# Optimization experiments

Measured on AMD Instinct MI355X. Metric: run time of the kernel, lower is better.

## Reference

```python
import jax, jax.numpy as jnp
import numpy as np

N_NODES = 50000
N_EDGES = 800000
DIM = 128
BN_EPS = 1e-5  # torch.nn.BatchNorm1d default


def _lin_init(k, fan_in, fan_out):
    kw, kb = jax.random.split(k)
    s = 1.0 / np.sqrt(fan_in)
    W = jax.random.uniform(kw, (fan_in, fan_out), jnp.float32, -s, s)
    b = jax.random.uniform(kb, (fan_out,), jnp.float32, -s, s)
    return W, b


def setup_inputs() -> dict:
    key = jax.random.key(0)
    ks = jax.random.split(key, 8)
    d = {}
    d['h'] = jax.random.normal(ks[0], (N_NODES, DIM), jnp.float32)
    d['e'] = jax.random.normal(ks[1], (N_EDGES, DIM), jnp.float32)
    d['src'] = jax.random.randint(ks[2], (N_EDGES,), 0, N_NODES)
    d['dst'] = jax.random.randint(ks[3], (N_EDGES,), 0, N_NODES)
    # mlp_atom: Linear(128,128) -> ReLU -> Linear(128,128)
    d['Wa1'], d['ba1'] = _lin_init(ks[4], DIM, DIM)
    d['Wa2'], d['ba2'] = _lin_init(ks[5], DIM, DIM)
    # mlp_bond
    d['Wb1'], d['bb1'] = _lin_init(ks[6], DIM, DIM)
    d['Wb2'], d['bb2'] = _lin_init(ks[7], DIM, DIM)
    # BatchNorm1d affine params
    d['gamma_a'] = jnp.ones((DIM,), jnp.float32)
    d['beta_a'] = jnp.zeros((DIM,), jnp.float32)
    d['gamma_b'] = jnp.ones((DIM,), jnp.float32)
    d['beta_b'] = jnp.zeros((DIM,), jnp.float32)
    return d


def _mlp(x, W1, b1, W2, b2):
    return jax.nn.relu(x @ W1 + b1) @ W2 + b2


def _bn(x, gamma, beta):
    # training-mode batch norm over the node/edge axis
    mu = jnp.mean(x, axis=0)
    var = jnp.var(x, axis=0)
    return (x - mu) * jax.lax.rsqrt(var + BN_EPS) * gamma + beta


def reference(h, e, src, dst, Wa1, ba1, Wa2, ba2, Wb1, bb1, Wb2, bb2,
              gamma_a, beta_a, gamma_b, beta_b):
    # --- bond (edge) update: GIN-style sum of endpoint atom feats + bond feat
    me = h[src] + h[dst] + e                      # [E, D] irregular gather
    e_new = _bn(_mlp(me, Wb1, bb1, Wb2, bb2), gamma_b, beta_b)
    e_new = e_new + e                             # residual (dropout=Identity)
    # --- atom (node) update: sum-aggregate incident bond feats
    agg = jax.ops.segment_sum(e_new, dst, num_segments=N_NODES)  # [N, D] scatter
    h_new = _bn(_mlp(h + agg, Wa1, ba1, Wa2, ba2), gamma_a, beta_a)
    h_new = h_new + h                             # residual
    return h_new, e_new
```

## Files before the change

kernel.cpp:

```cpp
#include <hip/hip_runtime.h>
#include <hip/hip_fp16.h>
#include <cstddef>

#define NN 50000
#define NE 800000
#define D 128
#define BN_EPS 1e-5f

typedef __attribute__((ext_vector_type(8))) short bf16x8;
typedef __attribute__((ext_vector_type(4))) float f32x4;
typedef __attribute__((ext_vector_type(4))) unsigned short us4;

__device__ __forceinline__ unsigned short f2bf(float x) {
    unsigned u = __float_as_uint(x);
    return (unsigned short)((u + 0x7fffu + ((u >> 16) & 1u)) >> 16);
}
__device__ __forceinline__ float bf2f(unsigned short b) {
    return __uint_as_float(((unsigned)b) << 16);
}

__global__ __launch_bounds__(256) void wprep_kernel(
    const float* __restrict__ W, unsigned short* __restrict__ Wt)
{
    const int idx = blockIdx.x * 256 + threadIdx.x;
    const int j  = idx & 7;
    const int l  = (idx >> 3) & 63;
    const int ks = (idx >> 9) & 3;
    const int ct = (idx >> 11) & 7;
    const int n  = 16 * ct + (l & 15);
    const int k  = 32 * ks + ((l >> 4) << 3) + j;
    Wt[idx] = f2bf(W[k * 128 + n]);
}

template<int MODE, int HALFX>
__global__ __launch_bounds__(256, 2) void mlp_mfma_kernel(
    const float* __restrict__ h, const float* __restrict__ e_or_agg,
    const int* __restrict__ src, const int* __restrict__ dst,
    const unsigned short* __restrict__ Wt1, const float* __restrict__ b1,
    const unsigned short* __restrict__ Wt2, const float* __restrict__ b2,
    void* __restrict__ x2out_v, float* __restrict__ stats)
{
    __shared__ __align__(16) unsigned short Xh[8192];
    __shared__ __align__(16) unsigned short Xl[8192];
    __shared__ __align__(16) float OUTB[64 * 132];

    const int tid  = threadIdx.x;
    const int lane = tid & 63;
    const int w    = tid >> 6;
    const int cg   = tid & 31;
    const int rg   = tid >> 5;
    const int c0   = cg * 4;
    const long r0  = (long)blockIdx.x * 64;

    const bf16x8* Wg1 = (const bf16x8*)Wt1;
    bf16x8 wf[8][4];
#pragma unroll
    for (int ct = 0; ct < 8; ++ct)
#pragma unroll
        for (int ks = 0; ks < 4; ++ks)
            wf[ct][ks] = Wg1[(ct * 4 + ks) * 64 + lane];

#pragma unroll
    for (int p = 0; p < 8; ++p) {
        const int  row  = p * 8 + rg;
        const long grow = r0 + row;
        float4 v = make_float4(0.f, 0.f, 0.f, 0.f);
        if (MODE == 0) {
            const int sN = src[grow];
            const int dN = dst[grow];
            const float4 ev = *(const float4*)(e_or_agg + (size_t)grow * D + c0);
            const float4 hs = *(const float4*)(h + (size_t)sN * D + c0);
            const float4 hd = *(const float4*)(h + (size_t)dN * D + c0);
            v.x = ev.x + hs.x + hd.x; v.y = ev.y + hs.y + hd.y;
            v.z = ev.z + hs.z + hd.z; v.w = ev.w + hs.w + hd.w;
        } else {
            if (grow < NN) {
                const float4 hv = *(const float4*)(h + (size_t)grow * D + c0);
                const float4 av = *(const float4*)(e_or_agg + (size_t)grow * D + c0);
                v.x = hv.x + av.x; v.y = hv.y + av.y;
                v.z = hv.z + av.z; v.w = hv.w + av.w;
            }
        }
        us4 hi, lo;
        hi.x = f2bf(v.x); lo.x = f2bf(v.x - bf2f(hi.x));
        hi.y = f2bf(v.y); lo.y = f2bf(v.y - bf2f(hi.y));
        hi.z = f2bf(v.z); lo.z = f2bf(v.z - bf2f(hi.z));
        hi.w = f2bf(v.w); lo.w = f2bf(v.w - bf2f(hi.w));
        const int addr = row * 128 + (((c0 >> 3) ^ (row & 7)) << 3) + (c0 & 7);
        *(us4*)&Xh[addr] = hi;
        *(us4*)&Xl[addr] = lo;
    }
    __syncthreads();

    const int arow = 16 * w + (lane & 15);
    bf16x8 ah[4], al[4];
#pragma unroll
    for (int ks = 0; ks < 4; ++ks) {
        const int col0  = 32 * ks + ((lane >> 4) << 3);
        const int aaddr = arow * 128 + (((col0 >> 3) ^ (arow & 7)) << 3);
        ah[ks] = *(const bf16x8*)&Xh[aaddr];
        al[ks] = *(const bf16x8*)&Xl[aaddr];
    }
    f32x4 acc[8];
#pragma unroll
    for (int ct = 0; ct < 8; ++ct) acc[ct] = (f32x4){0.f, 0.f, 0.f, 0.f};
#pragma unroll
    for (int ct = 0; ct < 8; ++ct)
#pragma unroll
        for (int ks = 0; ks < 4; ++ks) {
            acc[ct] = __builtin_amdgcn_mfma_f32_16x16x32_bf16(ah[ks], wf[ct][ks], acc[ct], 0, 0, 0);
            acc[ct] = __builtin_amdgcn_mfma_f32_16x16x32_bf16(al[ks], wf[ct][ks], acc[ct], 0, 0, 0);
        }

    const bf16x8* Wg2 = (const bf16x8*)Wt2;
#pragma unroll
    for (int ct = 0; ct < 8; ++ct)
#pragma unroll
        for (int ks = 0; ks < 4; ++ks)
            wf[ct][ks] = Wg2[(ct * 4 + ks) * 64 + lane];

#pragma unroll
    for (int ct = 0; ct < 8; ++ct) {
        const float b1c = b1[16 * ct + (lane & 15)];
#pragma unroll
        for (int r = 0; r < 4; ++r) {
            const int row = 16 * w + ((lane >> 4) << 2) + r;
            OUTB[row * 132 + 16 * ct + (lane & 15)] = fmaxf(acc[ct][r] + b1c, 0.f);
        }
    }
    __syncthreads();

#pragma unroll
    for (int p = 0; p < 8; ++p) {
        const int row = p * 8 + rg;
        const float4 v = *(const float4*)&OUTB[row * 132 + c0];
        us4 hi, lo;
        hi.x = f2bf(v.x); lo.x = f2bf(v.x - bf2f(hi.x));
        hi.y = f2bf(v.y); lo.y = f2bf(v.y - bf2f(hi.y));
        hi.z = f2bf(v.z); lo.z = f2bf(v.z - bf2f(hi.z));
        hi.w = f2bf(v.w); lo.w = f2bf(v.w - bf2f(hi.w));
        const int addr = row * 128 + (((c0 >> 3) ^ (row & 7)) << 3) + (c0 & 7);
        *(us4*)&Xh[addr] = hi;
        *(us4*)&Xl[addr] = lo;
    }
    __syncthreads();

#pragma unroll
    for (int ks = 0; ks < 4; ++ks) {
        const int col0  = 32 * ks + ((lane >> 4) << 3);
        const int aaddr = arow * 128 + (((col0 >> 3) ^ (arow & 7)) << 3);
        ah[ks] = *(const bf16x8*)&Xh[aaddr];
        al[ks] = *(const bf16x8*)&Xl[aaddr];
    }
    f32x4 a2[8];
#pragma unroll
    for (int ct = 0; ct < 8; ++ct) a2[ct] = (f32x4){0.f, 0.f, 0.f, 0.f};
#pragma unroll
    for (int ct = 0; ct < 8; ++ct)
#pragma unroll
        for (int ks = 0; ks < 4; ++ks) {
            a2[ct] = __builtin_amdgcn_mfma_f32_16x16x32_bf16(ah[ks], wf[ct][ks], a2[ct], 0, 0, 0);
            a2[ct] = __builtin_amdgcn_mfma_f32_16x16x32_bf16(al[ks], wf[ct][ks], a2[ct], 0, 0, 0);
        }

#pragma unroll
    for (int ct = 0; ct < 8; ++ct) {
        const float b2c = b2[16 * ct + (lane & 15)];
#pragma unroll
        for (int r = 0; r < 4; ++r) {
            const int row = 16 * w + ((lane >> 4) << 2) + r;
            OUTB[row * 132 + 16 * ct + (lane & 15)] = a2[ct][r] + b2c;
        }
    }
    __syncthreads();

    float ts[4] = {0.f, 0.f, 0.f, 0.f};
    float tq[4] = {0.f, 0.f, 0.f, 0.f};
#pragma unroll
    for (int p = 0; p < 8; ++p) {
        const int  row  = p * 8 + rg;
        const long grow = r0 + row;
        if (MODE == 1 && grow >= NN) continue;
        const float4 v = *(const float4*)&OUTB[row * 132 + c0];
        if (HALFX) {
            __half* xp = (__half*)x2out_v + (size_t)grow * D + c0;
            *(__half2*)(xp)     = __floats2half2_rn(v.x, v.y);
            *(__half2*)(xp + 2) = __floats2half2_rn(v.z, v.w);
        } else {
            *(float4*)((float*)x2out_v + (size_t)grow * D + c0) = v;
        }
        ts[0] += v.x; ts[1] += v.y; ts[2] += v.z; ts[3] += v.w;
        tq[0] += v.x * v.x; tq[1] += v.y * v.y;
        tq[2] += v.z * v.z; tq[3] += v.w * v.w;
    }

    float* red = (float*)Xh;
    *(float4*)&red[rg * 128 + c0]        = make_float4(ts[0], ts[1], ts[2], ts[3]);
    *(float4*)&red[2048 + rg * 128 + c0] = make_float4(tq[0], tq[1], tq[2], tq[3]);
    __syncthreads();
    if (tid < 128) {
        float s = 0.f, q = 0.f;
#pragma unroll
        for (int g = 0; g < 8; ++g) {
            s += red[g * 128 + tid];
            q += red[2048 + g * 128 + tid];
        }
        unsafeAtomicAdd(&stats[tid], s);
        unsafeAtomicAdd(&stats[128 + tid], q);
    }
}

__global__ void bn_finalize_kernel(float* __restrict__ stats,
                                   const float* __restrict__ gamma,
                                   const float* __restrict__ beta,
                                   float inv_count)
{
    const int c = threadIdx.x;
    if (c < D) {
        const float mu  = stats[c] * inv_count;
        const float var = stats[128 + c] * inv_count - mu * mu;
        const float sc  = rsqrtf(var + BN_EPS) * gamma[c];
        stats[256 + c] = sc;
        stats[384 + c] = beta[c] - mu * sc;
    }
}

__global__ __launch_bounds__(256) void hist_kernel(
    const int* __restrict__ dst, int* __restrict__ cnt)
{
    const int i = blockIdx.x * 256 + threadIdx.x;
    if (i < NE) atomicAdd(&cnt[dst[i]], 1);
}

__global__ __launch_bounds__(1024) void scan_kernel(
    const int* __restrict__ cnt, int* __restrict__ off)
{
    __shared__ int part[1024];
    const int t = threadIdx.x;
    const int SEG = (NN + 1023) / 1024;
    const int base = t * SEG;

    int s = 0;
    for (int i = 0; i < SEG; ++i) {
        const int idx = base + i;
        if (idx < NN) s += cnt[idx];
    }
    part[t] = s;
    __syncthreads();
    for (int d = 1; d < 1024; d <<= 1) {
        int v = (t >= d) ? part[t - d] : 0;
        __syncthreads();
        part[t] += v;
        __syncthreads();
    }
    int run = (t > 0) ? part[t - 1] : 0;
    for (int i = 0; i < SEG; ++i) {
        const int idx = base + i;
        if (idx < NN) { off[idx] = run; run += cnt[idx]; }
    }
    if (t == 1023) off[NN] = part[1023];
}

__global__ __launch_bounds__(256) void csr_scatter_kernel(
    const int* __restrict__ dst, const int* __restrict__ off,
    int* __restrict__ cnt, int* __restrict__ csr)
{
    const int i = blockIdx.x * 256 + threadIdx.x;
    if (i < NE) {
        const int d = dst[i];
        const int p = atomicSub(&cnt[d], 1) - 1;
        csr[off[d] + p] = i;
    }
}

template<int HALFX>
__global__ __launch_bounds__(256) void apply_gather_kernel(
    const float* __restrict__ e, const float* __restrict__ stats,
    const int* __restrict__ off, const int* __restrict__ csr,
    const void* __restrict__ x2src, float* __restrict__ eout,
    float* __restrict__ agg)
{
    const int node = blockIdx.x * 4 + (threadIdx.x >> 6);
    const int lane = threadIdx.x & 63;
    const int c0   = lane * 2;
    if (node >= NN) return;

    const float2 sc = *(const float2*)(stats + 256 + c0);
    const float2 sh = *(const float2*)(stats + 384 + c0);
    float2 acc = make_float2(0.f, 0.f);
    const int jb = off[node], je = off[node + 1];
    int j = jb;
    for (; j + 2 <= je; j += 2) {
        const int e0 = csr[j];
        const int e1 = csr[j + 1];
        const size_t b0 = (size_t)e0 * D + c0;
        const size_t b1 = (size_t)e1 * D + c0;
        float2 x0, x1;
        if (HALFX) {
            x0 = __half22float2(*(const __half2*)((const __half*)x2src + b0));
            x1 = __half22float2(*(const __half2*)((const __half*)x2src + b1));
        } else {
            x0 = *(const float2*)(eout + b0);
            x1 = *(const float2*)(eout + b1);
        }
        const float2 ev0 = *(const float2*)(e + b0);
        const float2 ev1 = *(const float2*)(e + b1);
        float2 v0, v1;
        v0.x = fmaf(x0.x, sc.x, sh.x) + ev0.x;
        v0.y = fmaf(x0.y, sc.y, sh.y) + ev0.y;
        v1.x = fmaf(x1.x, sc.x, sh.x) + ev1.x;
        v1.y = fmaf(x1.y, sc.y, sh.y) + ev1.y;
        *(float2*)(eout + b0) = v0;
        *(float2*)(eout + b1) = v1;
        acc.x += v0.x + v1.x;
        acc.y += v0.y + v1.y;
    }
    if (j < je) {
        const int e0 = csr[j];
        const size_t b0 = (size_t)e0 * D + c0;
        float2 x0;
        if (HALFX) {
            x0 = __half22float2(*(const __half2*)((const __half*)x2src + b0));
        } else {
            x0 = *(const float2*)(eout + b0);
        }
        const float2 ev0 = *(const float2*)(e + b0);
        float2 v0;
        v0.x = fmaf(x0.x, sc.x, sh.x) + ev0.x;
        v0.y = fmaf(x0.y, sc.y, sh.y) + ev0.y;
        *(float2*)(eout + b0) = v0;
        acc.x += v0.x;
        acc.y += v0.y;
    }
    *(float2*)(agg + (size_t)node * D + c0) = acc;
}

__global__ __launch_bounds__(256) void node_apply_kernel(
    const float* __restrict__ h, const float* __restrict__ stats,
    float* __restrict__ hout)
{
    const int gid = blockIdx.x * 256 + threadIdx.x;
    const int c0  = (gid & 31) * 4;
    const size_t base = (size_t)(gid >> 5) * D + c0;

    const float4 sc = *(const float4*)(stats + 256 + c0);
    const float4 sh = *(const float4*)(stats + 384 + c0);
    const float4 x  = *(const float4*)(hout + base);
    const float4 hv = *(const float4*)(h + base);
    float4 v;
    v.x = fmaf(x.x, sc.x, sh.x) + hv.x;
    v.y = fmaf(x.y, sc.y, sh.y) + hv.y;
    v.z = fmaf(x.z, sc.z, sh.z) + hv.z;
    v.w = fmaf(x.w, sc.w, sh.w) + hv.w;
    *(float4*)(hout + base) = v;
}

extern "C" void kernel_launch(void* const* d_in, const int* in_sizes, int n_in,
                              void* d_out, int out_size, void* d_ws, size_t ws_size,
                              hipStream_t stream)
{
    const float* h   = (const float*)d_in[0];
    const float* e   = (const float*)d_in[1];
    const int*   src = (const int*)d_in[2];
    const int*   dst = (const int*)d_in[3];
    const float* Wa1 = (const float*)d_in[4];
    const float* ba1 = (const float*)d_in[5];
    const float* Wa2 = (const float*)d_in[6];
    const float* ba2 = (const float*)d_in[7];
    const float* Wb1 = (const float*)d_in[8];
    const float* bb1 = (const float*)d_in[9];
    const float* Wb2 = (const float*)d_in[10];
    const float* bb2 = (const float*)d_in[11];
    const float* ga  = (const float*)d_in[12];
    const float* bea = (const float*)d_in[13];
    const float* gb  = (const float*)d_in[14];
    const float* beb = (const float*)d_in[15];

    float* out  = (float*)d_out;
    float* hnew = out;
    float* enew = out + (size_t)NN * D;

    float* ws     = (float*)d_ws;
    float* estats = ws;
    float* nstats = ws + 512;
    int*   icnt   = (int*)(ws + 1024);
    int*   ioff   = icnt + NN;
    unsigned short* wtb1 = (unsigned short*)(ioff + NN + 1 + 3);
    unsigned short* wtb2 = wtb1 + 16384;
    unsigned short* wta1 = wtb2 + 16384;
    unsigned short* wta2 = wta1 + 16384;
    int*    icsr = (int*)(wta2 + 16384);
    float*  agg  = (float*)(icsr + NE);
    __half* x2h  = (__half*)(agg + (size_t)NN * D);
    const size_t need_half = (size_t)((char*)(x2h + (size_t)NE * D) - (char*)d_ws);
    const bool use_half = (ws_size >= need_half);

    hipMemsetAsync(d_ws, 0, (size_t)(1024 + NN) * sizeof(float), stream);

    wprep_kernel<<<64, 256, 0, stream>>>(Wb1, wtb1);
    wprep_kernel<<<64, 256, 0, stream>>>(Wb2, wtb2);
    wprep_kernel<<<64, 256, 0, stream>>>(Wa1, wta1);
    wprep_kernel<<<64, 256, 0, stream>>>(Wa2, wta2);

    hist_kernel<<<(NE + 255) / 256, 256, 0, stream>>>(dst, icnt);
    scan_kernel<<<1, 1024, 0, stream>>>(icnt, ioff);
    csr_scatter_kernel<<<(NE + 255) / 256, 256, 0, stream>>>(dst, ioff, icnt, icsr);

    if (use_half) {
        mlp_mfma_kernel<0, 1><<<NE / 64, 256, 0, stream>>>(
            h, e, src, dst, wtb1, bb1, wtb2, bb2, (void*)x2h, estats);
        bn_finalize_kernel<<<1, 128, 0, stream>>>(estats, gb, beb, 1.0f / NE);
        apply_gather_kernel<1><<<(NN + 3) / 4, 256, 0, stream>>>(
            e, estats, ioff, icsr, (const void*)x2h, enew, agg);
    } else {
        mlp_mfma_kernel<0, 0><<<NE / 64, 256, 0, stream>>>(
            h, e, src, dst, wtb1, bb1, wtb2, bb2, (void*)enew, estats);
        bn_finalize_kernel<<<1, 128, 0, stream>>>(estats, gb, beb, 1.0f / NE);
        apply_gather_kernel<0><<<(NN + 3) / 4, 256, 0, stream>>>(
            e, estats, ioff, icsr, nullptr, enew, agg);
    }

    mlp_mfma_kernel<1, 0><<<(NN + 63) / 64, 256, 0, stream>>>(
        h, agg, nullptr, nullptr, wta1, ba1, wta2, ba2, (void*)hnew, nstats);
    bn_finalize_kernel<<<1, 128, 0, stream>>>(nstats, ga, bea, 1.0f / NN);
    node_apply_kernel<<<(NN * 32) / 256, 256, 0, stream>>>(h, nstats, hnew);
}
```

Measured before the change: 802.9 us.

## Drop split-bf16 low part in MLP GEMMs and vectorize apply-gather with half-wave edges

The MLP kernel stops using the hi/lo bf16 split for activations, so each GEMM issues half as many MFMAs and the Xl shared buffer goes away. The smaller shared footprint lets the launch bound ask for 3 blocks per CU instead of 2. Separately, the apply/gather kernel now has each half-wave handle a different edge with float4 accesses and combines the two halves with a shuffle. Dropping the low bf16 part lowers activation precision to plain bf16, which may hurt accuracy against the fp32 reference.

New measurement: 977.0 us. 21.7% more time.

```diff
diff --git a/kernel.cpp b/kernel.cpp
--- a/kernel.cpp
+++ b/kernel.cpp
@@ -14,9 +14,6 @@
 __device__ __forceinline__ unsigned short f2bf(float x) {
     unsigned u = __float_as_uint(x);
     return (unsigned short)((u + 0x7fffu + ((u >> 16) & 1u)) >> 16);
-}
-__device__ __forceinline__ float bf2f(unsigned short b) {
-    return __uint_as_float(((unsigned)b) << 16);
 }
 
 __global__ __launch_bounds__(256) void wprep_kernel(
@@ -33,7 +30,7 @@
 }
 
 template<int MODE, int HALFX>
-__global__ __launch_bounds__(256, 2) void mlp_mfma_kernel(
+__global__ __launch_bounds__(256, 3) void mlp_mfma_kernel(
     const float* __restrict__ h, const float* __restrict__ e_or_agg,
     const int* __restrict__ src, const int* __restrict__ dst,
     const unsigned short* __restrict__ Wt1, const float* __restrict__ b1,
@@ -41,7 +38,6 @@
     void* __restrict__ x2out_v, float* __restrict__ stats)
 {
     __shared__ __align__(16) unsigned short Xh[8192];
-    __shared__ __align__(16) unsigned short Xl[8192];
     __shared__ __align__(16) float OUTB[64 * 132];
 
     const int tid  = threadIdx.x;
@@ -81,25 +77,21 @@
                 v.z = hv.z + av.z; v.w = hv.w + av.w;
             }
         }
-        us4 hi, lo;
-        hi.x = f2bf(v.x); lo.x = f2bf(v.x - bf2f(hi.x));
-        hi.y = f2bf(v.y); lo.y = f2bf(v.y - bf2f(hi.y));
-        hi.z = f2bf(v.z); lo.z = f2bf(v.z - bf2f(hi.z));
-        hi.w = f2bf(v.w); lo.w = f2bf(v.w - bf2f(hi.w));
+        us4 hi;
+        hi.x = f2bf(v.x); hi.y = f2bf(v.y);
+        hi.z = f2bf(v.z); hi.w = f2bf(v.w);
         const int addr = row * 128 + (((c0 >> 3) ^ (row & 7)) << 3) + (c0 & 7);
         *(us4*)&Xh[addr] = hi;
-        *(us4*)&Xl[addr] = lo;
     }
     __syncthreads();
 
     const int arow = 16 * w + (lane & 15);
-    bf16x8 ah[4], al[4];
+    bf16x8 ah[4];
 #pragma unroll
     for (int ks = 0; ks < 4; ++ks) {
         const int col0  = 32 * ks + ((lane >> 4) << 3);
         const int aaddr = arow * 128 + (((col0 >> 3) ^ (arow & 7)) << 3);
         ah[ks] = *(const bf16x8*)&Xh[aaddr];
-        al[ks] = *(const bf16x8*)&Xl[aaddr];
     }
     f32x4 acc[8];
 #pragma unroll
@@ -107,10 +99,8 @@
 #pragma unroll
     for (int ct = 0; ct < 8; ++ct)
 #pragma unroll
-        for (int ks = 0; ks < 4; ++ks) {
+        for (int ks = 0; ks < 4; ++ks)
             acc[ct] = __builtin_amdgcn_mfma_f32_16x16x32_bf16(ah[ks], wf[ct][ks], acc[ct], 0, 0, 0);
-            acc[ct] = __builtin_amdgcn_mfma_f32_16x16x32_bf16(al[ks], wf[ct][ks], acc[ct], 0, 0, 0);
-        }
 
     const bf16x8* Wg2 = (const bf16x8*)Wt2;
 #pragma unroll
@@ -134,14 +124,11 @@
     for (int p = 0; p < 8; ++p) {
         const int row = p * 8 + rg;
         const float4 v = *(const float4*)&OUTB[row * 132 + c0];
-        us4 hi, lo;
-        hi.x = f2bf(v.x); lo.x = f2bf(v.x - bf2f(hi.x));
-        hi.y = f2bf(v.y); lo.y = f2bf(v.y - bf2f(hi.y));
-        hi.z = f2bf(v.z); lo.z = f2bf(v.z - bf2f(hi.z));
-        hi.w = f2bf(v.w); lo.w = f2bf(v.w - bf2f(hi.w));
+        us4 hi;
+        hi.x = f2bf(v.x); hi.y = f2bf(v.y);
+        hi.z = f2bf(v.z); hi.w = f2bf(v.w);
         const int addr = row * 128 + (((c0 >> 3) ^ (row & 7)) << 3) + (c0 & 7);
         *(us4*)&Xh[addr] = hi;
-        *(us4*)&Xl[addr] = lo;
     }
     __syncthreads();
 
@@ -150,7 +137,6 @@
         const int col0  = 32 * ks + ((lane >> 4) << 3);
         const int aaddr = arow * 128 + (((col0 >> 3) ^ (arow & 7)) << 3);
         ah[ks] = *(const bf16x8*)&Xh[aaddr];
-        al[ks] = *(const bf16x8*)&Xl[aaddr];
     }
     f32x4 a2[8];
 #pragma unroll
@@ -158,10 +144,8 @@
 #pragma unroll
     for (int ct = 0; ct < 8; ++ct)
 #pragma unroll
-        for (int ks = 0; ks < 4; ++ks) {
+        for (int ks = 0; ks < 4; ++ks)
             a2[ct] = __builtin_amdgcn_mfma_f32_16x16x32_bf16(ah[ks], wf[ct][ks], a2[ct], 0, 0, 0);
-            a2[ct] = __builtin_amdgcn_mfma_f32_16x16x32_bf16(al[ks], wf[ct][ks], a2[ct], 0, 0, 0);
-        }
 
 #pragma unroll
     for (int ct = 0; ct < 8; ++ct) {
@@ -196,14 +180,14 @@
 
     float* red = (float*)Xh;
     *(float4*)&red[rg * 128 + c0]        = make_float4(ts[0], ts[1], ts[2], ts[3]);
-    *(float4*)&red[2048 + rg * 128 + c0] = make_float4(tq[0], tq[1], tq[2], tq[3]);
+    *(float4*)&red[1024 + rg * 128 + c0] = make_float4(tq[0], tq[1], tq[2], tq[3]);
     __syncthreads();
     if (tid < 128) {
         float s = 0.f, q = 0.f;
 #pragma unroll
         for (int g = 0; g < 8; ++g) {
             s += red[g * 128 + tid];
-            q += red[2048 + g * 128 + tid];
+            q += red[1024 + g * 128 + tid];
         }
         unsafeAtomicAdd(&stats[tid], s);
         unsafeAtomicAdd(&stats[128 + tid], q);
@@ -282,57 +266,48 @@
 {
     const int node = blockIdx.x * 4 + (threadIdx.x >> 6);
     const int lane = threadIdx.x & 63;
-    const int c0   = lane * 2;
+    const int half = lane >> 5;
+    const int c0   = (lane & 31) * 4;
     if (node >= NN) return;
 
-    const float2 sc = *(const float2*)(stats + 256 + c0);
-    const float2 sh = *(const float2*)(stats + 384 + c0);
-    float2 acc = make_float2(0.f, 0.f);
+    const float4 sc = *(const float4*)(stats + 256 + c0);
+    const float4 sh = *(const float4*)(stats + 384 + c0);
+    float4 acc = make_float4(0.f, 0.f, 0.f, 0.f);
     const int jb = off[node], je = off[node + 1];
-    int j = jb;
-    for (; j + 2 <= je; j += 2) {
-        const int e0 = csr[j];
-        const int e1 = csr[j + 1];
-        const size_t b0 = (size_t)e0 * D + c0;
-        const size_t b1 = (size_t)e1 * D + c0;
-        float2 x0, x1;
-        if (HALFX) {
-            x0 = __half22float2(*(const __half2*)((const __half*)x2src + b0));
-            x1 = __half22float2(*(const __half2*)((const __half*)x2src + b1));
-        } else {
-            x0 = *(const float2*)(eout + b0);
-            x1 = *(const float2*)(eout + b1);
-        }
-        const float2 ev0 = *(const float2*)(e + b0);
-        const float2 ev1 = *(const float2*)(e + b1);
-        float2 v0, v1;
-        v0.x = fmaf(x0.x, sc.x, sh.x) + ev0.x;
-        v0.y = fmaf(x0.y, sc.y, sh.y) + ev0.y;
-        v1.x = fmaf(x1.x, sc.x, sh.x) + ev1.x;
-        v1.y = fmaf(x1.y, sc.y, sh.y) + ev1.y;
-        *(float2*)(eout + b0) = v0;
-        *(float2*)(eout + b1) = v1;
-        acc.x += v0.x + v1.x;
-        acc.y += v0.y + v1.y;
-    }
-    if (j < je) {
-        const int e0 = csr[j];
-        const size_t b0 = (size_t)e0 * D + c0;
-        float2 x0;
-        if (HALFX) {
-            x0 = __half22float2(*(const __half2*)((const __half*)x2src + b0));
-        } else {
-            x0 = *(const float2*)(eout + b0);
-        }
-        const float2 ev0 = *(const float2*)(e + b0);
-        float2 v0;
-        v0.x = fmaf(x0.x, sc.x, sh.x) + ev0.x;
-        v0.y = fmaf(x0.y, sc.y, sh.y) + ev0.y;
-        *(float2*)(eout + b0) = v0;
-        acc.x += v0.x;
-        acc.y += v0.y;
-    }
-    *(float2*)(agg + (size_t)node * D + c0) = acc;
+    const int niter = (je - jb + 1) >> 1;
+
+#pragma unroll 2
+    for (int p = 0; p < niter; ++p) {
+        const int j0 = jb + 2 * p + half;
+        if (j0 < je) {
+            const int eidx = csr[j0];
+            const size_t base = (size_t)eidx * D + c0;
+            float4 x;
+            if (HALFX) {
+                const int2 xi = *(const int2*)((const __half*)x2src + base);
+                const float2 f0 = __half22float2(*(const __half2*)&xi.x);
+                const float2 f1 = __half22float2(*(const __half2*)&xi.y);
+                x = make_float4(f0.x, f0.y, f1.x, f1.y);
+            } else {
+                x = *(const float4*)(eout + base);
+            }
+            const float4 ev = *(const float4*)(e + base);
+            float4 v;
+            v.x = fmaf(x.x, sc.x, sh.x) + ev.x;
+            v.y = fmaf(x.y, sc.y, sh.y) + ev.y;
+            v.z = fmaf(x.z, sc.z, sh.z) + ev.z;
+            v.w = fmaf(x.w, sc.w, sh.w) + ev.w;
+            *(float4*)(eout + base) = v;
+            acc.x += v.x; acc.y += v.y; acc.z += v.z; acc.w += v.w;
+        }
+    }
+
+    acc.x += __shfl_xor(acc.x, 32);
+    acc.y += __shfl_xor(acc.y, 32);
+    acc.z += __shfl_xor(acc.z, 32);
+    acc.w += __shfl_xor(acc.w, 32);
+    if (half == 0)
+        *(float4*)(agg + (size_t)node * D + c0) = acc;
 }
 
 __global__ __launch_bounds__(256) void node_apply_kernel(
```
